# Performance work log

Hardware: AMD Instinct MI355X
Metric: run time of the kernel (lower is better)

Reference implementation:

```python
import jax, jax.numpy as jnp
import numpy as np

P = 64       # number of pathways
NV = 512     # features per pathway (nvar[i])
W = 256      # hidden width per pathway
COV = 16     # covariates
B = 2048     # batch
EPS = 1e-5   # BatchNorm eps
SLOPE = 0.2  # LeakyReLU negative slope


def _lrelu(v):
    return jnp.where(v >= 0, v, SLOPE * v)


def setup_inputs() -> dict:
    key = jax.random.key(0)
    ks = jax.random.split(key, 8)
    x = jax.random.normal(ks[0], (B, P * NV + COV), dtype=jnp.float32)
    # per-pathway weights (no bias), stacked across pathways -> grouped GEMM
    W1 = jax.random.normal(ks[1], (P, NV, W), dtype=jnp.float32) * (1.0 / np.sqrt(NV))
    W2 = jax.random.normal(ks[2], (P, W, W), dtype=jnp.float32) * (1.0 / np.sqrt(W))
    W3 = jax.random.normal(ks[3], (P, W), dtype=jnp.float32) * (1.0 / np.sqrt(W))
    gamma = jnp.ones((P,), dtype=jnp.float32)   # bn_path weight
    beta = jnp.zeros((P,), dtype=jnp.float32)   # bn_path bias
    fc_w = jax.random.normal(ks[4], (P + COV, 1), dtype=jnp.float32) * 0.05
    fc_b = jnp.full((1,), 0.001, dtype=jnp.float32)
    return {"x": x, "W1": W1, "W2": W2, "W3": W3,
            "gamma": gamma, "beta": beta, "fc_w": fc_w, "fc_b": fc_b}


def reference(x, W1, W2, W3, gamma, beta, fc_w, fc_b):
    # pathway blocks (dropout = identity in eval): grouped GEMMs over P pathways
    xp = x[:, : P * NV].reshape(B, P, NV)
    h = _lrelu(jnp.einsum('bpi,pio->bpo', xp, W1))
    h = _lrelu(jnp.einsum('bpi,pio->bpo', h, W2))
    p = _lrelu(jnp.einsum('bpi,pi->bp', h, W3))          # [B, P]
    # BatchNorm1d (training-mode batch statistics, biased variance)
    mean = p.mean(axis=0)
    var = p.var(axis=0)
    pn = (p - mean) / jnp.sqrt(var + EPS) * gamma + beta
    # global L2 (Frobenius) normalization, as torch.norm(pathway_layer, 2)
    pn = pn / jnp.linalg.norm(pn)
    # concat covariates, final linear + sigmoid
    z = jnp.concatenate([pn, x[:, P * NV: P * NV + COV]], axis=1)  # [B, P+COV]
    return jax.nn.sigmoid(z @ fc_w + fc_b)                         # [B, 1]
```

## Files before the change

### kernel.cpp

```cpp
#include <hip/hip_runtime.h>
#include <hip/hip_bf16.h>

#define PW 64
#define NV 512
#define HW 256
#define COV 16
#define BATCH 2048
#define XROW (PW * NV + COV)

typedef short s16x8 __attribute__((ext_vector_type(8)));
typedef float f32x4 __attribute__((ext_vector_type(4)));

__device__ __forceinline__ unsigned short f2bf(float f) {
    union { float f; unsigned int u; } v;
    v.f = f;
    unsigned int u = v.u;
    unsigned int r = (u + 0x7fffu + ((u >> 16) & 1u)) >> 16;
    return (unsigned short)r;
}

__device__ __forceinline__ unsigned int pack2(float a, float b) {
    __hip_bfloat162 h = __float22bfloat162_rn(float2{a, b});
    union { __hip_bfloat162 h; unsigned int u; } c;
    c.h = h;
    return c.u;
}

__device__ __forceinline__ float lrelu(float v) { return v >= 0.f ? v : 0.2f * v; }

__global__ __launch_bounds__(256)
void transpose_all(const float* __restrict__ W1, const float* __restrict__ W2,
                   unsigned short* __restrict__ W1T, unsigned short* __restrict__ W2T) {
    __shared__ float tile[32][33];
    const float* in;
    unsigned short* out;
    int R, C, c0, r0, p;
    int bx = blockIdx.x;
    if (bx < 8192) {
        R = NV; C = HW;
        c0 = (bx & 7) * 32;
        r0 = ((bx >> 3) & 15) * 32;
        p  = bx >> 7;
        in = W1; out = W1T;
    } else {
        bx -= 8192;
        R = HW; C = HW;
        c0 = (bx & 7) * 32;
        r0 = ((bx >> 3) & 7) * 32;
        p  = bx >> 6;
        in = W2; out = W2T;
    }
    const float* ip = in + (size_t)p * R * C;
    unsigned short* op = out + (size_t)p * R * C;
    const int tx = threadIdx.x & 31;
    const int ty = threadIdx.x >> 5;
    #pragma unroll
    for (int j = 0; j < 32; j += 8)
        tile[ty + j][tx] = ip[(size_t)(r0 + ty + j) * C + c0 + tx];
    __syncthreads();
    #pragma unroll
    for (int j = 0; j < 32; j += 8)
        op[(size_t)(c0 + ty + j) * R + r0 + tx] = f2bf(tile[tx][ty + j]);
}

__global__ __launch_bounds__(256, 2)
void pathway_fused(const float* __restrict__ x, const unsigned short* __restrict__ W1T,
                   const unsigned short* __restrict__ W2T, const float* __restrict__ W3,
                   float* __restrict__ pvec) {
    __shared__ __align__(16) unsigned short As[64][72];
    __shared__ __align__(16) unsigned short Bs[256][72];
    __shared__ __align__(16) unsigned short H1t[64][264];
    __shared__ float red[4][64];

    const int bm0 = blockIdx.x * 64;
    const int p   = blockIdx.y;
    const int t    = threadIdx.x;
    const int lane = t & 63;
    const int wave = t >> 6;
    const int wn   = wave * 64;
    const int l15  = lane & 15;
    const int quad = lane >> 4;

    const float* Ap          = x   + (size_t)p * NV;
    const unsigned short* B1 = W1T + (size_t)p * HW * NV;
    const unsigned short* B2 = W2T + (size_t)p * HW * HW;

    {
        f32x4 acc[4][4] = {};
        for (int k0 = 0; k0 < NV; k0 += 64) {
            #pragma unroll
            for (int i = 0; i < 4; ++i) {
                int idx = t + i * 256;
                int row = idx >> 4;
                int c4  = (idx & 15) * 4;
                float4 v = *(const float4*)(Ap + (size_t)(bm0 + row) * XROW + k0 + c4);
                uint2 u;
                u.x = pack2(v.x, v.y);
                u.y = pack2(v.z, v.w);
                *(uint2*)&As[row][c4] = u;
            }
            #pragma unroll
            for (int i = 0; i < 8; ++i) {
                int idx = t + i * 256;
                int row = idx >> 3;
                int c8  = (idx & 7) * 8;
                *(s16x8*)&Bs[row][c8] = *(const s16x8*)(B1 + (size_t)row * NV + k0 + c8);
            }
            __syncthreads();
            #pragma unroll
            for (int kk = 0; kk < 64; kk += 32) {
                s16x8 af[4], bfr[4];
                #pragma unroll
                for (int mi = 0; mi < 4; ++mi)
                    af[mi] = *(const s16x8*)&As[mi * 16 + l15][kk + quad * 8];
                #pragma unroll
                for (int ni = 0; ni < 4; ++ni)
                    bfr[ni] = *(const s16x8*)&Bs[wn + ni * 16 + l15][kk + quad * 8];
                #pragma unroll
                for (int mi = 0; mi < 4; ++mi)
                    #pragma unroll
                    for (int ni = 0; ni < 4; ++ni)
                        acc[mi][ni] = __builtin_amdgcn_mfma_f32_16x16x32_bf16(
                            af[mi], bfr[ni], acc[mi][ni], 0, 0, 0);
            }
            __syncthreads();
        }
        #pragma unroll
        for (int mi = 0; mi < 4; ++mi)
            #pragma unroll
            for (int ni = 0; ni < 4; ++ni)
                #pragma unroll
                for (int r = 0; r < 4; ++r)
                    H1t[mi * 16 + quad * 4 + r][wn + ni * 16 + l15] =
                        f2bf(lrelu(acc[mi][ni][r]));
    }
    __syncthreads();

    f32x4 acc2[4][4] = {};
    for (int k0 = 0; k0 < HW; k0 += 64) {
        #pragma unroll
        for (int i = 0; i < 8; ++i) {
            int idx = t + i * 256;
            int row = idx >> 3;
            int c8  = (idx & 7) * 8;
            *(s16x8*)&Bs[row][c8] = *(const s16x8*)(B2 + (size_t)row * HW + k0 + c8);
        }
        __syncthreads();
        #pragma unroll
        for (int kk = 0; kk < 64; kk += 32) {
            s16x8 af[4], bfr[4];
            #pragma unroll
            for (int mi = 0; mi < 4; ++mi)
                af[mi] = *(const s16x8*)&H1t[mi * 16 + l15][k0 + kk + quad * 8];
            #pragma unroll
            for (int ni = 0; ni < 4; ++ni)
                bfr[ni] = *(const s16x8*)&Bs[wn + ni * 16 + l15][kk + quad * 8];
            #pragma unroll
            for (int mi = 0; mi < 4; ++mi)
                #pragma unroll
                for (int ni = 0; ni < 4; ++ni)
                    acc2[mi][ni] = __builtin_amdgcn_mfma_f32_16x16x32_bf16(
                        af[mi], bfr[ni], acc2[mi][ni], 0, 0, 0);
        }
        __syncthreads();
    }

    float w3v[4];
    #pragma unroll
    for (int ni = 0; ni < 4; ++ni)
        w3v[ni] = W3[(size_t)p * HW + wn + ni * 16 + l15];
    float part[4][4];
    #pragma unroll
    for (int mi = 0; mi < 4; ++mi) {
        #pragma unroll
        for (int r = 0; r < 4; ++r) {
            float s = 0.f;
            #pragma unroll
            for (int ni = 0; ni < 4; ++ni)
                s += lrelu(acc2[mi][ni][r]) * w3v[ni];
            part[mi][r] = s;
        }
    }
    #pragma unroll
    for (int off = 1; off < 16; off <<= 1)
        #pragma unroll
        for (int mi = 0; mi < 4; ++mi)
            #pragma unroll
            for (int r = 0; r < 4; ++r)
                part[mi][r] += __shfl_xor(part[mi][r], off);
    if (l15 == 0)
        #pragma unroll
        for (int mi = 0; mi < 4; ++mi)
            #pragma unroll
            for (int r = 0; r < 4; ++r)
                red[wave][mi * 16 + quad * 4 + r] = part[mi][r];
    __syncthreads();
    if (t < 64) {
        float s = red[0][t] + red[1][t] + red[2][t] + red[3][t];
        pvec[(size_t)p * BATCH + bm0 + t] = lrelu(s);
    }
}

__global__ __launch_bounds__(256)
void stats_k(const float* __restrict__ pvec, float* __restrict__ stat) {
    const int p = blockIdx.x;
    float s = 0.f, q = 0.f;
    for (int i = threadIdx.x; i < BATCH; i += 256) {
        float v = pvec[(size_t)p * BATCH + i];
        s += v; q += v * v;
    }
    #pragma unroll
    for (int off = 32; off; off >>= 1) {
        s += __shfl_down(s, off);
        q += __shfl_down(q, off);
    }
    __shared__ float ls[4], lq[4];
    const int wave = threadIdx.x >> 6, lane = threadIdx.x & 63;
    if (lane == 0) { ls[wave] = s; lq[wave] = q; }
    __syncthreads();
    if (threadIdx.x == 0) {
        float S = ls[0] + ls[1] + ls[2] + ls[3];
        float Q = lq[0] + lq[1] + lq[2] + lq[3];
        float mean = S * (1.f / BATCH);
        float var  = Q * (1.f / BATCH) - mean * mean;
        stat[p]       = mean;
        stat[64 + p]  = rsqrtf(var + 1e-5f);
        stat[128 + p] = var;
    }
}

__global__ __launch_bounds__(256)
void final_k(const float* __restrict__ pvec, const float* __restrict__ stat,
             const float* __restrict__ gamma, const float* __restrict__ beta,
             const float* __restrict__ x, const float* __restrict__ fc_w,
             const float* __restrict__ fc_b, float* __restrict__ out) {
    const int b = blockIdx.x * 256 + threadIdx.x;
    float nsq = 0.f;
    #pragma unroll
    for (int p = 0; p < PW; ++p) {
        float g = gamma[p], bt = beta[p], var = stat[128 + p], inv = stat[64 + p];
        nsq += (float)BATCH * (g * g * var * inv * inv + bt * bt);
    }
    const float rn = rsqrtf(nsq);
    float acc = fc_b[0];
    #pragma unroll
    for (int p = 0; p < PW; ++p) {
        float pn = (pvec[(size_t)p * BATCH + b] - stat[p]) * stat[64 + p] * gamma[p] + beta[p];
        acc += pn * rn * fc_w[p];
    }
    #pragma unroll
    for (int c = 0; c < COV; ++c)
        acc += x[(size_t)b * XROW + PW * NV + c] * fc_w[PW + c];
    out[b] = 1.f / (1.f + __expf(-acc));
}

extern "C" void kernel_launch(void* const* d_in, const int* in_sizes, int n_in,
                              void* d_out, int out_size, void* d_ws, size_t ws_size,
                              hipStream_t stream) {
    const float* x     = (const float*)d_in[0];
    const float* W1    = (const float*)d_in[1];
    const float* W2    = (const float*)d_in[2];
    const float* W3    = (const float*)d_in[3];
    const float* gamma = (const float*)d_in[4];
    const float* beta  = (const float*)d_in[5];
    const float* fc_w  = (const float*)d_in[6];
    const float* fc_b  = (const float*)d_in[7];
    float* out = (float*)d_out;

    char* ws = (char*)d_ws;
    size_t off = 0;
    unsigned short* W1T = (unsigned short*)(ws + off); off += (size_t)PW * NV * HW * 2;
    unsigned short* W2T = (unsigned short*)(ws + off); off += (size_t)PW * HW * HW * 2;
    float* pvec = (float*)(ws + off); off += (size_t)PW * BATCH * 4;
    float* stat = (float*)(ws + off); off += 256 * 4;

    transpose_all<<<dim3(8192 + 4096), 256, 0, stream>>>(W1, W2, W1T, W2T);

    pathway_fused<<<dim3(BATCH / 64, PW), 256, 0, stream>>>(x, W1T, W2T, W3, pvec);

    stats_k<<<PW, 256, 0, stream>>>(pvec, stat);

    final_k<<<BATCH / 256, 256, 0, stream>>>(pvec, stat, gamma, beta, x, fc_w, fc_b, out);
}
```

Before: 462.2 us.

## Pre-swizzle weight tiles and load them via global_load_lds with XCD-aware block mapping

```diff
diff --git a/kernel.cpp b/kernel.cpp
--- a/kernel.cpp
+++ b/kernel.cpp
@@ -7,6 +7,7 @@
 #define COV 16
 #define BATCH 2048
 #define XROW (PW * NV + COV)
+#define IMG 16384
 
 typedef short s16x8 __attribute__((ext_vector_type(8)));
 typedef float f32x4 __attribute__((ext_vector_type(4)));
@@ -28,53 +29,66 @@
 
 __device__ __forceinline__ float lrelu(float v) { return v >= 0.f ? v : 0.2f * v; }
 
+__device__ __forceinline__ void gl_lds16(const void* g, void* l) {
+    __builtin_amdgcn_global_load_lds(
+        (const __attribute__((address_space(1))) void*)g,
+        (__attribute__((address_space(3))) void*)l, 16, 0, 0);
+}
+
 __global__ __launch_bounds__(256)
 void transpose_all(const float* __restrict__ W1, const float* __restrict__ W2,
-                   unsigned short* __restrict__ W1T, unsigned short* __restrict__ W2T) {
-    __shared__ float tile[32][33];
-    const float* in;
-    unsigned short* out;
-    int R, C, c0, r0, p;
+                   unsigned short* __restrict__ W1I, unsigned short* __restrict__ W2I) {
+    __shared__ float tile[64][260];
     int bx = blockIdx.x;
-    if (bx < 8192) {
-        R = NV; C = HW;
-        c0 = (bx & 7) * 32;
-        r0 = ((bx >> 3) & 15) * 32;
-        p  = bx >> 7;
-        in = W1; out = W1T;
+    const float* src;
+    unsigned short* dst;
+    if (bx < 512) {
+        int p = bx >> 3, kb = bx & 7;
+        src = W1 + ((size_t)p * NV + kb * 64) * HW;
+        dst = W1I + (size_t)(p * 8 + kb) * IMG;
     } else {
-        bx -= 8192;
-        R = HW; C = HW;
-        c0 = (bx & 7) * 32;
-        r0 = ((bx >> 3) & 7) * 32;
-        p  = bx >> 6;
-        in = W2; out = W2T;
-    }
-    const float* ip = in + (size_t)p * R * C;
-    unsigned short* op = out + (size_t)p * R * C;
-    const int tx = threadIdx.x & 31;
-    const int ty = threadIdx.x >> 5;
-    #pragma unroll
-    for (int j = 0; j < 32; j += 8)
-        tile[ty + j][tx] = ip[(size_t)(r0 + ty + j) * C + c0 + tx];
+        bx -= 512;
+        int p = bx >> 2, kb = bx & 3;
+        src = W2 + ((size_t)p * HW + kb * 64) * HW;
+        dst = W2I + (size_t)(p * 4 + kb) * IMG;
+    }
+    const int t = threadIdx.x;
+    #pragma unroll
+    for (int i = 0; i < 16; ++i) {
+        int idx = t + i * 256;
+        int r = idx >> 6, c4 = (idx & 63) << 2;
+        *(float4*)&tile[r][c4] = *(const float4*)(src + (size_t)r * HW + c4);
+    }
     __syncthreads();
     #pragma unroll
-    for (int j = 0; j < 32; j += 8)
-        op[(size_t)(c0 + ty + j) * R + r0 + tx] = f2bf(tile[tx][ty + j]);
+    for (int pass = 0; pass < 8; ++pass) {
+        int idx = pass * 256 + t;
+        int n = idx >> 3, s = idx & 7;
+        int g = s ^ (n & 7);
+        unsigned short v[8];
+        #pragma unroll
+        for (int j = 0; j < 8; ++j)
+            v[j] = f2bf(tile[g * 8 + j][n]);
+        *(s16x8*)(dst + (size_t)idx * 8) = *(s16x8*)v;
+    }
 }
 
 __global__ __launch_bounds__(256, 2)
-void pathway_fused(const float* __restrict__ x, const unsigned short* __restrict__ W1T,
-                   const unsigned short* __restrict__ W2T, const float* __restrict__ W3,
+void pathway_fused(const float* __restrict__ x, const unsigned short* __restrict__ W1I,
+                   const unsigned short* __restrict__ W2I, const float* __restrict__ W3,
                    float* __restrict__ pvec) {
     __shared__ __align__(16) unsigned short As[64][72];
-    __shared__ __align__(16) unsigned short Bs[256][72];
+    __shared__ __align__(16) unsigned short Bs[256 * 64];
     __shared__ __align__(16) unsigned short H1t[64][264];
     __shared__ float red[4][64];
 
-    const int bm0 = blockIdx.x * 64;
-    const int p   = blockIdx.y;
-    const int t    = threadIdx.x;
+    const int lin = blockIdx.x + blockIdx.y * (BATCH / 64);
+    const int xcd = lin & 7;
+    const int idx0 = lin >> 3;
+    const int p   = xcd * 8 + (idx0 >> 5);
+    const int bm0 = (idx0 & 31) * 64;
+
+    const int t = threadIdx.x;
     const int lane = t & 63;
     const int wave = t >> 6;
     const int wn   = wave * 64;
@@ -82,31 +96,42 @@
     const int quad = lane >> 4;
 
     const float* Ap          = x   + (size_t)p * NV;
-    const unsigned short* B1 = W1T + (size_t)p * HW * NV;
-    const unsigned short* B2 = W2T + (size_t)p * HW * HW;
+    const unsigned short* B1 = W1I + (size_t)p * 8 * IMG;
+    const unsigned short* B2 = W2I + (size_t)p * 4 * IMG;
 
     {
+        float4 aReg[4];
+        #pragma unroll
+        for (int i = 0; i < 4; ++i) {
+            int ii = t + i * 256, row = ii >> 4, c4 = (ii & 15) * 4;
+            aReg[i] = *(const float4*)(Ap + (size_t)(bm0 + row) * XROW + c4);
+        }
         f32x4 acc[4][4] = {};
         for (int k0 = 0; k0 < NV; k0 += 64) {
             #pragma unroll
             for (int i = 0; i < 4; ++i) {
-                int idx = t + i * 256;
-                int row = idx >> 4;
-                int c4  = (idx & 15) * 4;
-                float4 v = *(const float4*)(Ap + (size_t)(bm0 + row) * XROW + k0 + c4);
+                int ii = t + i * 256, row = ii >> 4, c4 = (ii & 15) * 4;
                 uint2 u;
-                u.x = pack2(v.x, v.y);
-                u.y = pack2(v.z, v.w);
+                u.x = pack2(aReg[i].x, aReg[i].y);
+                u.y = pack2(aReg[i].z, aReg[i].w);
                 *(uint2*)&As[row][c4] = u;
             }
-            #pragma unroll
-            for (int i = 0; i < 8; ++i) {
-                int idx = t + i * 256;
-                int row = idx >> 3;
-                int c8  = (idx & 7) * 8;
-                *(s16x8*)&Bs[row][c8] = *(const s16x8*)(B1 + (size_t)row * NV + k0 + c8);
+            {
+                const unsigned short* img = B1 + (size_t)(k0 >> 6) * IMG;
+                #pragma unroll
+                for (int c = 0; c < 8; ++c) {
+                    int off = wave * 8192 + c * 1024;
+                    gl_lds16((const char*)img + off + lane * 16, (char*)Bs + off);
+                }
             }
             __syncthreads();
+            if (k0 + 64 < NV) {
+                #pragma unroll
+                for (int i = 0; i < 4; ++i) {
+                    int ii = t + i * 256, row = ii >> 4, c4 = (ii & 15) * 4;
+                    aReg[i] = *(const float4*)(Ap + (size_t)(bm0 + row) * XROW + k0 + 64 + c4);
+                }
+            }
             #pragma unroll
             for (int kk = 0; kk < 64; kk += 32) {
                 s16x8 af[4], bfr[4];
@@ -114,8 +139,11 @@
                 for (int mi = 0; mi < 4; ++mi)
                     af[mi] = *(const s16x8*)&As[mi * 16 + l15][kk + quad * 8];
                 #pragma unroll
-                for (int ni = 0; ni < 4; ++ni)
-                    bfr[ni] = *(const s16x8*)&Bs[wn + ni * 16 + l15][kk + quad * 8];
+                for (int ni = 0; ni < 4; ++ni) {
+                    int row  = wn + ni * 16 + l15;
+                    int slot = ((kk >> 3) + quad) ^ (row & 7);
+                    bfr[ni] = *(const s16x8*)&Bs[row * 64 + slot * 8];
+                }
                 #pragma unroll
                 for (int mi = 0; mi < 4; ++mi)
                     #pragma unroll
@@ -138,12 +166,11 @@
 
     f32x4 acc2[4][4] = {};
     for (int k0 = 0; k0 < HW; k0 += 64) {
-        #pragma unroll
-        for (int i = 0; i < 8; ++i) {
-            int idx = t + i * 256;
-            int row = idx >> 3;
-            int c8  = (idx & 7) * 8;
-            *(s16x8*)&Bs[row][c8] = *(const s16x8*)(B2 + (size_t)row * HW + k0 + c8);
+        const unsigned short* img = B2 + (size_t)(k0 >> 6) * IMG;
+        #pragma unroll
+        for (int c = 0; c < 8; ++c) {
+            int off = wave * 8192 + c * 1024;
+            gl_lds16((const char*)img + off + lane * 16, (char*)Bs + off);
         }
         __syncthreads();
         #pragma unroll
@@ -153,8 +180,11 @@
             for (int mi = 0; mi < 4; ++mi)
                 af[mi] = *(const s16x8*)&H1t[mi * 16 + l15][k0 + kk + quad * 8];
             #pragma unroll
-            for (int ni = 0; ni < 4; ++ni)
-                bfr[ni] = *(const s16x8*)&Bs[wn + ni * 16 + l15][kk + quad * 8];
+            for (int ni = 0; ni < 4; ++ni) {
+                int row  = wn + ni * 16 + l15;
+                int slot = ((kk >> 3) + quad) ^ (row & 7);
+                bfr[ni] = *(const s16x8*)&Bs[row * 64 + slot * 8];
+            }
             #pragma unroll
             for (int mi = 0; mi < 4; ++mi)
                 #pragma unroll
@@ -269,14 +299,14 @@
 
     char* ws = (char*)d_ws;
     size_t off = 0;
-    unsigned short* W1T = (unsigned short*)(ws + off); off += (size_t)PW * NV * HW * 2;
-    unsigned short* W2T = (unsigned short*)(ws + off); off += (size_t)PW * HW * HW * 2;
+    unsigned short* W1I = (unsigned short*)(ws + off); off += (size_t)PW * NV * HW * 2;
+    unsigned short* W2I = (unsigned short*)(ws + off); off += (size_t)PW * HW * HW * 2;
     float* pvec = (float*)(ws + off); off += (size_t)PW * BATCH * 4;
     float* stat = (float*)(ws + off); off += 256 * 4;
 
-    transpose_all<<<dim3(8192 + 4096), 256, 0, stream>>>(W1, W2, W1T, W2T);
-
-    pathway_fused<<<dim3(BATCH / 64, PW), 256, 0, stream>>>(x, W1T, W2T, W3, pvec);
+    transpose_all<<<dim3(512 + 256), 256, 0, stream>>>(W1, W2, W1I, W2I);
+
+    pathway_fused<<<dim3(BATCH / 64, PW), 256, 0, stream>>>(x, W1I, W2I, W3, pvec);
 
     stats_k<<<PW, 256, 0, stream>>>(pvec, stat);
 
```

Result: slower. 480.2 us (+3.9%).
